# Performance work log

Hardware: AMD Instinct MI355X
Metric: run time of the kernel (lower is better)

## Reference

```python
import jax, jax.numpy as jnp
import numpy as np

N_TOKENS = 4096
HIDDEN = 1024
N_EXPERTS = 8
TOP_K = 2
EXPANDED = 2048


def setup_inputs() -> dict:
    key = jax.random.key(0)
    ks = jax.random.split(key, 4)
    tokens = jax.random.normal(ks[0], (N_TOKENS, HIDDEN), dtype=jnp.float32)
    router_w = jax.random.normal(ks[1], (N_EXPERTS, HIDDEN), dtype=jnp.float32) * (1.0 / np.sqrt(HIDDEN))
    router_b = jnp.zeros((N_EXPERTS,), dtype=jnp.float32)
    w1 = jax.random.normal(ks[2], (N_EXPERTS, HIDDEN, EXPANDED), dtype=jnp.float32) * (1.0 / np.sqrt(HIDDEN))
    b1 = jnp.zeros((N_EXPERTS, EXPANDED), dtype=jnp.float32)
    w2 = jax.random.normal(ks[3], (N_EXPERTS, EXPANDED, HIDDEN), dtype=jnp.float32) * (1.0 / np.sqrt(EXPANDED))
    b2 = jnp.zeros((N_EXPERTS, HIDDEN), dtype=jnp.float32)
    return {"tokens": tokens, "router_w": router_w, "router_b": router_b,
            "w1": w1, "b1": b1, "w2": w2, "b2": b2}


def reference(tokens, router_w, router_b, w1, b1, w2, b2):
    # Router: logits [N, E], top-k scores -> softmax over the k selected experts.
    logits = tokens @ router_w.T + router_b
    top_scores, expert_ids = jax.lax.top_k(logits, TOP_K)      # [N, K]
    probs = jax.nn.softmax(top_scores, axis=-1)                # [N, K]

    # Instead of gathering full per-token weight matrices (as the torch code does),
    # run each expert's dense MLP over all tokens and combine with the per-token
    # routing weight for that expert. Identical math: each token's contribution is
    # sum_k probs[n,k] * MLP_{expert_ids[n,k]}(tokens[n]).
    out = jnp.zeros_like(tokens)
    for e in range(N_EXPERTS):
        h = jax.nn.gelu(tokens @ w1[e] + b1[e], approximate=False)  # [N, EXPANDED]
        o = h @ w2[e] + b2[e]                                       # [N, HIDDEN]
        # Combined routing weight for expert e (top_k indices are distinct).
        gate = jnp.sum(jnp.where(expert_ids == e, probs, 0.0), axis=-1)  # [N]
        out = out + gate[:, None] * o
    return out
```

## Files before the change

kernel.cpp:

```cpp
#include <hip/hip_runtime.h>
#include <hip/hip_bf16.h>

typedef unsigned short u16;
typedef __attribute__((ext_vector_type(8))) short short8;
typedef __attribute__((ext_vector_type(4))) float f32x4;

#define N_TOKENS 4096
#define HIDDEN   1024
#define N_EXP    8
#define EXPAND   2048

#define TOKB_OFF  0ull
#define W1T_OFF   8388608ull
#define OBUF_OFF  8388608ull
#define W2T_OFF   41943040ull
#define H_OFF     75497472ull
#define RLT_OFF   109051904ull
#define RLG_OFF   109084672ull
#define CNT_OFF   109117440ull
#define E01_OFF   109117472ull
#define GATE_OFF  109183008ull
#define ROWS2_OFF 109215776ull

__device__ __forceinline__ u16 f2bf(float f) {
  union { float f; unsigned u; } v; v.f = f;
  unsigned r = v.u + 0x7fffu + ((v.u >> 16) & 1u);
  return (u16)(r >> 16);
}

__device__ __forceinline__ void glds16(const void* g, void* l) {
  __builtin_amdgcn_global_load_lds(
      (const __attribute__((address_space(1))) void*)g,
      (__attribute__((address_space(3))) void*)l, 16, 0, 0);
}

__device__ __forceinline__ float gelu_tanh(float x) {
  float u = x * (0.7978845608f + 0.0356774081f * x * x);
  float t = __expf(-2.0f * fabsf(u));
  float th = (1.0f - t) / (1.0f + t);
  th = (u >= 0.0f) ? th : -th;
  return 0.5f * x * (1.0f + th);
}

__global__ __launch_bounds__(256) void cvt_transpose_k(const float* __restrict__ in,
                                                       u16* __restrict__ out,
                                                       int R, int C) {
  __shared__ float t[32][33];
  int e = blockIdx.z;
  int r0 = blockIdx.y * 32, c0 = blockIdx.x * 32;
  const float* ip = in + (size_t)e * R * C;
  u16* op = out + (size_t)e * R * C;
  int tx = threadIdx.x, ty = threadIdx.y;
  #pragma unroll
  for (int i = 0; i < 4; ++i)
    t[ty + i * 8][tx] = ip[(size_t)(r0 + ty + i * 8) * C + c0 + tx];
  __syncthreads();
  #pragma unroll
  for (int i = 0; i < 4; ++i)
    op[(size_t)(c0 + ty + i * 8) * R + r0 + tx] = f2bf(t[tx][ty + i * 8]);
}

__global__ __launch_bounds__(256) void logits_k(const float* __restrict__ tokens,
                                                const float* __restrict__ rw,
                                                const float* __restrict__ rb,
                                                u16* __restrict__ tokb,
                                                int* __restrict__ e01,
                                                float* __restrict__ gates) {
  __shared__ float rwl[N_EXP * HIDDEN];
  int tid = threadIdx.x;
  for (int i = tid; i < N_EXP * HIDDEN; i += 256) rwl[i] = rw[i];
  __syncthreads();
  int w = tid >> 6, l = tid & 63;
  int t = blockIdx.x * 4 + w;
  const float* tp = tokens + (size_t)t * HIDDEN;
  u16* tb = tokb + (size_t)t * HIDDEN;
  float acc[8] = {0.f,0.f,0.f,0.f,0.f,0.f,0.f,0.f};
  for (int k = l; k < HIDDEN; k += 64) {
    float tv = tp[k];
    tb[k] = f2bf(tv);
    #pragma unroll
    for (int e = 0; e < 8; ++e) acc[e] += tv * rwl[e * HIDDEN + k];
  }
  #pragma unroll
  for (int off = 32; off >= 1; off >>= 1) {
    #pragma unroll
    for (int e = 0; e < 8; ++e) acc[e] += __shfl_xor(acc[e], off);
  }
  if (l == 0) {
    float lg[8];
    #pragma unroll
    for (int e = 0; e < 8; ++e) lg[e] = acc[e] + rb[e];
    int b0 = 0; float v0 = lg[0];
    #pragma unroll
    for (int e = 1; e < 8; ++e) if (lg[e] > v0) { v0 = lg[e]; b0 = e; }
    int b1 = -1; float v1 = -3.4e38f;
    #pragma unroll
    for (int e = 0; e < 8; ++e) {
      if (e == b0) continue;
      if (lg[e] > v1) { v1 = lg[e]; b1 = e; }
    }
    float d = expf(v1 - v0);
    float p1 = d / (1.f + d);
    float p0 = 1.f - p1;
    e01[t * 2] = b0;   e01[t * 2 + 1] = b1;
    gates[t * 2] = p0; gates[t * 2 + 1] = p1;
  }
}

__global__ __launch_bounds__(1024) void order_k(const int* __restrict__ e01,
                                                const float* __restrict__ gates,
                                                int* __restrict__ cnt,
                                                int* __restrict__ rlt,
                                                float* __restrict__ rlg,
                                                int* __restrict__ rows2) {
  __shared__ int slotbuf[2 * N_TOKENS];
  __shared__ int wcnt[16][N_EXP];
  __shared__ int base_run[N_EXP];
  __shared__ int basep[N_EXP];
  int tid = threadIdx.x, w = tid >> 6, l = tid & 63;
  if (tid < N_EXP) base_run[tid] = 0;
  __syncthreads();
  unsigned long long ltmask = (1ull << l) - 1ull;
  #pragma unroll
  for (int c = 0; c < 8; ++c) {
    int i = c * 1024 + tid;
    int ei = e01[i];
    int myrank = 0;
    #pragma unroll
    for (int e = 0; e < N_EXP; ++e) {
      unsigned long long b = __ballot(ei == e);
      if (l == 0) wcnt[w][e] = __popcll(b);
      if (ei == e) myrank = __popcll(b & ltmask);
    }
    __syncthreads();
    if (tid < N_EXP) {
      int e = tid, off = base_run[e];
      #pragma unroll
      for (int ww = 0; ww < 16; ++ww) {
        int v = wcnt[ww][e]; wcnt[ww][e] = off; off += v;
      }
      base_run[e] = off;
    }
    __syncthreads();
    slotbuf[i] = wcnt[w][ei] + myrank;
    __syncthreads();
  }
  if (tid < N_EXP) cnt[tid] = base_run[tid];
  if (tid == 0) {
    int s = 0;
    for (int e = 0; e < N_EXP; ++e) { basep[e] = s; s += base_run[e]; }
  }
  __syncthreads();
  #pragma unroll
  for (int c = 0; c < 8; ++c) {
    int i = c * 1024 + tid;
    int e = e01[i];
    int row = basep[e] + slotbuf[i];
    rlt[row] = i >> 1;
    rlg[row] = gates[i];
    rows2[i] = row;
  }
}


#define STAGE(Ad, Bd, KT) {                                                      \
  _Pragma("unroll") for (int c = 0; c < 4; ++c)                                  \
    glds16(ga[c] + (size_t)(KT) * 64, &Ad[(c * 256 + threadIdx.x) * 8]);         \
  _Pragma("unroll") for (int c = 0; c < 2; ++c)                                  \
    glds16(gb[c] + (size_t)(KT) * 64, &Bd[(c * 256 + threadIdx.x) * 8]);         \
}

#define GEMM_TILE(As, Bs) {                                                      \
  _Pragma("unroll") for (int kk = 0; kk < 2; ++kk) {                             \
    short8 afr[4], bfr[2];                                                       \
    _Pragma("unroll") for (int i = 0; i < 4; ++i)                                \
      afr[i] = *(const short8*)&As[oa[kk][i]];                                   \
    _Pragma("unroll") for (int j = 0; j < 2; ++j)                                \
      bfr[j] = *(const short8*)&Bs[ob[kk][j]];                                   \
    _Pragma("unroll") for (int i = 0; i < 4; ++i)                                \
      _Pragma("unroll") for (int j = 0; j < 2; ++j)                              \
        acc[i][j] = __builtin_amdgcn_mfma_f32_16x16x32_bf16(                     \
            afr[i], bfr[j], acc[i][j], 0, 0, 0);                                 \
  }                                                                              \
}

#define FRAG_OFFSETS {                                                           \
  _Pragma("unroll") for (int kk = 0; kk < 2; ++kk) {                             \
    int cc = kk * 4 + lg;                                                        \
    _Pragma("unroll") for (int i = 0; i < 4; ++i) {                              \
      int Ra = wr * 64 + i * 16 + lr;                                            \
      oa[kk][i] = Ra * 64 + (cc ^ (Ra & 7)) * 8;                                 \
    }                                                                            \
    _Pragma("unroll") for (int j = 0; j < 2; ++j) {                              \
      int Rb = wc * 32 + j * 16 + lr;                                            \
      ob[kk][j] = Rb * 64 + (cc ^ (Rb & 7)) * 8;                                 \
    }                                                                            \
  }                                                                              \
}

__global__ __launch_bounds__(256) void ffn1_k(const u16* __restrict__ tok,
                                              const u16* __restrict__ w1t,
                                              const float* __restrict__ b1,
                                              const int* __restrict__ rlt,
                                              const int* __restrict__ cnt,
                                              u16* __restrict__ h) {
  __shared__ __align__(16) short A0[8192];
  __shared__ __align__(16) short A1[8192];
  __shared__ __align__(16) short B0[4096];
  __shared__ __align__(16) short B1[4096];

  int tid = threadIdx.x, w = tid >> 6, l = tid & 63;
  int wr = w >> 1, wc = w & 1;
  int lr = l & 15, lg = l >> 4;
  int oa[2][4], ob[2][2];
  FRAG_OFFSETS

  int cl[8];
  #pragma unroll
  for (int i = 0; i < 8; ++i) cl[i] = cnt[i];
  int NTm = 0;
  #pragma unroll
  for (int i = 0; i < 8; ++i) NTm += (cl[i] + 127) >> 7;
  int NT = NTm * (EXPAND / 64);

  for (int idx = blockIdx.x; idx < NT; idx += gridDim.x) {
    int g = idx >> 5, nt = idx & 31;
    int e = 0, m0 = 0, ne = 0, mtb = 0, at = 0, ar = 0;
    #pragma unroll
    for (int i = 0; i < 8; ++i) {
      int ti = (cl[i] + 127) >> 7;
      bool sel = (g >= at) && (g < at + ti);
      if (sel) { e = i; mtb = at; m0 = ar; ne = cl[i]; }
      at += ti; ar += cl[i];
    }
    int mt = g - mtb;
    int m0g = m0 + mt * 128;
    int mrem = ne - mt * 128;

    const u16* ga[4]; const u16* gb[2];
    #pragma unroll
    for (int c = 0; c < 4; ++c) {
      int flat = c * 256 + tid, rih = flat >> 3;
      int ch = (flat & 7) ^ (rih & 7);
      int tokid = rlt[m0g + ((rih < mrem) ? rih : 0)];
      ga[c] = tok + (size_t)tokid * HIDDEN + ch * 8;
    }
    #pragma unroll
    for (int c = 0; c < 2; ++c) {
      int flat = c * 256 + tid, rih = flat >> 3;
      int ch = (flat & 7) ^ (rih & 7);
      int nrow = nt * 64 + rih;
      gb[c] = w1t + (size_t)e * (EXPAND * HIDDEN) + (size_t)nrow * HIDDEN + ch * 8;
    }

    f32x4 acc[4][2] = {};
    STAGE(A0, B0, 0)
    __syncthreads();
    #pragma unroll 1
    for (int it = 0; it < 8; ++it) {
      STAGE(A1, B1, 2 * it + 1)
      GEMM_TILE(A0, B0)
      __syncthreads();
      if (it < 7) STAGE(A0, B0, 2 * it + 2)
      GEMM_TILE(A1, B1)
      __syncthreads();
    }

    #pragma unroll
    for (int i = 0; i < 4; ++i) {
      #pragma unroll
      for (int r = 0; r < 4; ++r) {
        int row = wr * 64 + i * 16 + lg * 4 + r;
        if (row >= mrem) continue;
        size_t hrow = (size_t)(m0g + row) * EXPAND;
        #pragma unroll
        for (int j = 0; j < 2; ++j) {
          int col = nt * 64 + wc * 32 + j * 16 + lr;
          float x = acc[i][j][r] + b1[e * EXPAND + col];
          h[hrow + col] = f2bf(gelu_tanh(x));
        }
      }
    }
  }
}

__global__ __launch_bounds__(256) void ffn2_k(const u16* __restrict__ h,
                                              const u16* __restrict__ w2t,
                                              const float* __restrict__ b2,
                                              const float* __restrict__ rlg,
                                              const int* __restrict__ cnt,
                                              float* __restrict__ obuf) {
  __shared__ __align__(16) short A0[8192];
  __shared__ __align__(16) short A1[8192];
  __shared__ __align__(16) short B0[4096];
  __shared__ __align__(16) short B1[4096];

  int tid = threadIdx.x, w = tid >> 6, l = tid & 63;
  int wr = w >> 1, wc = w & 1;
  int lr = l & 15, lg = l >> 4;
  int oa[2][4], ob[2][2];
  FRAG_OFFSETS

  int cl[8];
  #pragma unroll
  for (int i = 0; i < 8; ++i) cl[i] = cnt[i];
  int NTm = 0;
  #pragma unroll
  for (int i = 0; i < 8; ++i) NTm += (cl[i] + 127) >> 7;
  int NT = NTm * (HIDDEN / 64);

  for (int idx = blockIdx.x; idx < NT; idx += gridDim.x) {
    int g = idx >> 4, nt = idx & 15;
    int e = 0, m0 = 0, ne = 0, mtb = 0, at = 0, ar = 0;
    #pragma unroll
    for (int i = 0; i < 8; ++i) {
      int ti = (cl[i] + 127) >> 7;
      bool sel = (g >= at) && (g < at + ti);
      if (sel) { e = i; mtb = at; m0 = ar; ne = cl[i]; }
      at += ti; ar += cl[i];
    }
    int mt = g - mtb;
    int m0g = m0 + mt * 128;
    int mrem = ne - mt * 128;

    const u16* ga[4]; const u16* gb[2];
    #pragma unroll
    for (int c = 0; c < 4; ++c) {
      int flat = c * 256 + tid, rih = flat >> 3;
      int ch = (flat & 7) ^ (rih & 7);
      int rowg = m0g + ((rih < mrem) ? rih : 0);
      ga[c] = h + (size_t)rowg * EXPAND + ch * 8;
    }
    #pragma unroll
    for (int c = 0; c < 2; ++c) {
      int flat = c * 256 + tid, rih = flat >> 3;
      int ch = (flat & 7) ^ (rih & 7);
      int nrow = nt * 64 + rih;
      gb[c] = w2t + (size_t)e * (HIDDEN * EXPAND) + (size_t)nrow * EXPAND + ch * 8;
    }

    f32x4 acc[4][2] = {};
    STAGE(A0, B0, 0)
    __syncthreads();
    #pragma unroll 1
    for (int it = 0; it < 16; ++it) {
      STAGE(A1, B1, 2 * it + 1)
      GEMM_TILE(A0, B0)
      __syncthreads();
      if (it < 15) STAGE(A0, B0, 2 * it + 2)
      GEMM_TILE(A1, B1)
      __syncthreads();
    }

    #pragma unroll
    for (int i = 0; i < 4; ++i) {
      #pragma unroll
      for (int r = 0; r < 4; ++r) {
        int row = wr * 64 + i * 16 + lg * 4 + r;
        if (row >= mrem) continue;
        float gate = rlg[m0g + row];
        size_t orow = (size_t)(m0g + row) * HIDDEN;
        #pragma unroll
        for (int j = 0; j < 2; ++j) {
          int col = nt * 64 + wc * 32 + j * 16 + lr;
          obuf[orow + col] = (acc[i][j][r] + b2[e * HIDDEN + col]) * gate;
        }
      }
    }
  }
}

__global__ __launch_bounds__(256) void combine_k(const float* __restrict__ obuf,
                                                 const int* __restrict__ rows2,
                                                 float* __restrict__ out) {
  int t = blockIdx.x, c = threadIdx.x;
  int r0 = rows2[t * 2], r1 = rows2[t * 2 + 1];
  float4 a = ((const float4*)obuf)[(size_t)r0 * 256 + c];
  float4 b = ((const float4*)obuf)[(size_t)r1 * 256 + c];
  float4 o;
  o.x = a.x + b.x; o.y = a.y + b.y; o.z = a.z + b.z; o.w = a.w + b.w;
  ((float4*)out)[(size_t)t * 256 + c] = o;
}

extern "C" void kernel_launch(void* const* d_in, const int* in_sizes, int n_in,
                              void* d_out, int out_size, void* d_ws, size_t ws_size,
                              hipStream_t stream) {
  const float* tokens   = (const float*)d_in[0];
  const float* router_w = (const float*)d_in[1];
  const float* router_b = (const float*)d_in[2];
  const float* w1       = (const float*)d_in[3];
  const float* b1       = (const float*)d_in[4];
  const float* w2       = (const float*)d_in[5];
  const float* b2       = (const float*)d_in[6];
  float* out = (float*)d_out;

  char* ws = (char*)d_ws;
  u16*   tokb  = (u16*)(ws + TOKB_OFF);
  u16*   w1t   = (u16*)(ws + W1T_OFF);
  float* obuf  = (float*)(ws + OBUF_OFF);
  u16*   w2t   = (u16*)(ws + W2T_OFF);
  u16*   h     = (u16*)(ws + H_OFF);
  int*   rlt   = (int*)(ws + RLT_OFF);
  float* rlg   = (float*)(ws + RLG_OFF);
  int*   cnt   = (int*)(ws + CNT_OFF);
  int*   e01   = (int*)(ws + E01_OFF);
  float* gates = (float*)(ws + GATE_OFF);
  int*   rows2 = (int*)(ws + ROWS2_OFF);

  cvt_transpose_k<<<dim3(EXPAND / 32, HIDDEN / 32, N_EXP), dim3(32, 8), 0, stream>>>(
      w1, w1t, HIDDEN, EXPAND);
  cvt_transpose_k<<<dim3(HIDDEN / 32, EXPAND / 32, N_EXP), dim3(32, 8), 0, stream>>>(
      w2, w2t, EXPAND, HIDDEN);
  logits_k<<<N_TOKENS / 4, 256, 0, stream>>>(tokens, router_w, router_b, tokb, e01, gates);
  order_k<<<1, 1024, 0, stream>>>(e01, gates, cnt, rlt, rlg, rows2);
  ffn1_k<<<2048, 256, 0, stream>>>(tokb, w1t, b1, rlt, cnt, h);
  ffn2_k<<<2048, 256, 0, stream>>>(h, w2t, b2, rlg, cnt, obuf);
  combine_k<<<N_TOKENS, 256, 0, stream>>>(obuf, rows2, out);
}
```

Measured before the change: 227.2 us.

## Assign blocks to experts round-robin instead of flattened tile index

Result: faster. 220.6 us (-2.9%).

```diff
diff --git a/kernel.cpp b/kernel.cpp
--- a/kernel.cpp
+++ b/kernel.cpp
@@ -215,25 +215,18 @@
   int oa[2][4], ob[2][2];
   FRAG_OFFSETS
 
-  int cl[8];
-  #pragma unroll
-  for (int i = 0; i < 8; ++i) cl[i] = cnt[i];
-  int NTm = 0;
-  #pragma unroll
-  for (int i = 0; i < 8; ++i) NTm += (cl[i] + 127) >> 7;
-  int NT = NTm * (EXPAND / 64);
-
-  for (int idx = blockIdx.x; idx < NT; idx += gridDim.x) {
-    int g = idx >> 5, nt = idx & 31;
-    int e = 0, m0 = 0, ne = 0, mtb = 0, at = 0, ar = 0;
-    #pragma unroll
-    for (int i = 0; i < 8; ++i) {
-      int ti = (cl[i] + 127) >> 7;
-      bool sel = (g >= at) && (g < at + ti);
-      if (sel) { e = i; mtb = at; m0 = ar; ne = cl[i]; }
-      at += ti; ar += cl[i];
-    }
-    int mt = g - mtb;
+  int e = blockIdx.x & 7;
+  int rnk = blockIdx.x >> 3;
+  int estr = gridDim.x >> 3;
+  int m0 = 0;
+  #pragma unroll
+  for (int i = 0; i < 8; ++i) { int ci = cnt[i]; if (i < e) m0 += ci; }
+  int ne = cnt[e];
+  int mts = (ne + 127) >> 7;
+  int NT_e = mts * (EXPAND / 64);
+
+  for (int r = rnk; r < NT_e; r += estr) {
+    int mt = r >> 5, nt = r & 31;
     int m0g = m0 + mt * 128;
     int mrem = ne - mt * 128;
 
@@ -269,14 +262,14 @@
     #pragma unroll
     for (int i = 0; i < 4; ++i) {
       #pragma unroll
-      for (int r = 0; r < 4; ++r) {
-        int row = wr * 64 + i * 16 + lg * 4 + r;
+      for (int rr = 0; rr < 4; ++rr) {
+        int row = wr * 64 + i * 16 + lg * 4 + rr;
         if (row >= mrem) continue;
         size_t hrow = (size_t)(m0g + row) * EXPAND;
         #pragma unroll
         for (int j = 0; j < 2; ++j) {
           int col = nt * 64 + wc * 32 + j * 16 + lr;
-          float x = acc[i][j][r] + b1[e * EXPAND + col];
+          float x = acc[i][j][rr] + b1[e * EXPAND + col];
           h[hrow + col] = f2bf(gelu_tanh(x));
         }
       }
@@ -301,25 +294,18 @@
   int oa[2][4], ob[2][2];
   FRAG_OFFSETS
 
-  int cl[8];
-  #pragma unroll
-  for (int i = 0; i < 8; ++i) cl[i] = cnt[i];
-  int NTm = 0;
-  #pragma unroll
-  for (int i = 0; i < 8; ++i) NTm += (cl[i] + 127) >> 7;
-  int NT = NTm * (HIDDEN / 64);
-
-  for (int idx = blockIdx.x; idx < NT; idx += gridDim.x) {
-    int g = idx >> 4, nt = idx & 15;
-    int e = 0, m0 = 0, ne = 0, mtb = 0, at = 0, ar = 0;
-    #pragma unroll
-    for (int i = 0; i < 8; ++i) {
-      int ti = (cl[i] + 127) >> 7;
-      bool sel = (g >= at) && (g < at + ti);
-      if (sel) { e = i; mtb = at; m0 = ar; ne = cl[i]; }
-      at += ti; ar += cl[i];
-    }
-    int mt = g - mtb;
+  int e = blockIdx.x & 7;
+  int rnk = blockIdx.x >> 3;
+  int estr = gridDim.x >> 3;
+  int m0 = 0;
+  #pragma unroll
+  for (int i = 0; i < 8; ++i) { int ci = cnt[i]; if (i < e) m0 += ci; }
+  int ne = cnt[e];
+  int mts = (ne + 127) >> 7;
+  int NT_e = mts * (HIDDEN / 64);
+
+  for (int r = rnk; r < NT_e; r += estr) {
+    int mt = r >> 4, nt = r & 15;
     int m0g = m0 + mt * 128;
     int mrem = ne - mt * 128;
 
@@ -355,15 +341,15 @@
     #pragma unroll
     for (int i = 0; i < 4; ++i) {
       #pragma unroll
-      for (int r = 0; r < 4; ++r) {
-        int row = wr * 64 + i * 16 + lg * 4 + r;
+      for (int rr = 0; rr < 4; ++rr) {
+        int row = wr * 64 + i * 16 + lg * 4 + rr;
         if (row >= mrem) continue;
         float gate = rlg[m0g + row];
         size_t orow = (size_t)(m0g + row) * HIDDEN;
         #pragma unroll
         for (int j = 0; j < 2; ++j) {
           int col = nt * 64 + wc * 32 + j * 16 + lr;
-          obuf[orow + col] = (acc[i][j][r] + b2[e * HIDDEN + col]) * gate;
+          obuf[orow + col] = (acc[i][j][rr] + b2[e * HIDDEN + col]) * gate;
         }
       }
     }
```
